# Optimization experiments

Hardware: AMD Instinct MI355X
Metric: run time of the kernel (lower is better)

## Reference

```python
import jax, jax.numpy as jnp
import numpy as np
from jax import lax

NUM_ITER = 10
SMOOTH = 1.0
CL_WEIGHT = 0.5


def _min_pool(x, wh, ww):
    # torch: -max_pool2d(-x) pads with -inf -> min-pool with +inf boundary
    return lax.reduce_window(x, jnp.inf, lax.min,
                             (1, 1, wh, ww), (1, 1, 1, 1),
                             [(0, 0), (0, 0), (wh // 2, wh // 2), (ww // 2, ww // 2)])


def _max_pool(x, wh, ww):
    return lax.reduce_window(x, -jnp.inf, lax.max,
                             (1, 1, wh, ww), (1, 1, 1, 1),
                             [(0, 0), (0, 0), (wh // 2, wh // 2), (ww // 2, ww // 2)])


def soft_erode(img):
    return jnp.minimum(_min_pool(img, 3, 1), _min_pool(img, 1, 3))


def soft_dilate(img):
    return _max_pool(img, 3, 3)


def soft_open(img):
    return soft_dilate(soft_erode(img))


def soft_skeleton(img, num_iter=NUM_ITER):
    # img: (B,1,H,W)
    skel = jax.nn.relu(img - soft_open(img))

    def body(i, carry):
        img_e, skel = carry
        img_e = soft_erode(img_e)
        delta = jax.nn.relu(img_e - soft_open(img_e))
        skel = skel + jax.nn.relu(delta - skel * delta)
        return (img_e, skel)

    _, skel = lax.fori_loop(0, num_iter, body, (img, skel))
    return skel


def soft_dice(pred, target, smooth=SMOOTH):
    inter = jnp.sum(pred * target)
    return (2.0 * inter + smooth) / (jnp.sum(pred) + jnp.sum(target) + smooth)


def setup_inputs() -> dict:
    key = jax.random.key(0)
    k1, k2 = jax.random.split(key)
    pred = jax.random.normal(k1, (8, 1, 1024, 1024), dtype=jnp.float32)
    target = jax.random.randint(k2, (8, 1, 1024, 1024), 0, 2, dtype=jnp.int32)
    return {"pred": pred, "target": target}


def reference(pred, target):
    pred_prob = jax.nn.sigmoid(pred)          # (B,1,H,W)
    target_f = target.astype(pred_prob.dtype)

    skel_pred = soft_skeleton(pred_prob)
    skel_target = soft_skeleton(target_f)

    tprec = (jnp.sum(skel_pred * target_f) + SMOOTH) / (jnp.sum(skel_pred) + SMOOTH)
    tsens = (jnp.sum(skel_target * pred_prob) + SMOOTH) / (jnp.sum(skel_target) + SMOOTH)
    cl_dice = 2.0 * tprec * tsens / (tprec + tsens + 1e-7)

    dice = soft_dice(pred_prob, target_f)
    combined = (1.0 - CL_WEIGHT) * dice + CL_WEIGHT * cl_dice
    loss = 1.0 - combined
    return loss
```

## Files before the change

### kernel.cpp

```cpp
#include <hip/hip_runtime.h>
#include <math.h>

#define IMG  1024
#define TILE 64
#define HALO 12
#define SPP  52
#define NPRED (90*SPP)
#define SEN2 0x40004000u

typedef _Float16 h2 __attribute__((ext_vector_type(2)));
union UH { unsigned u; h2 h; };
__device__ __forceinline__ h2 u2h(unsigned u){ UH x; x.u=u; return x.h; }
__device__ __forceinline__ unsigned h2u(h2 h){ UH x; x.h=h; return x.u; }
__device__ __forceinline__ h2 pmin(h2 a, h2 b){ return __builtin_elementwise_min(a,b); }
__device__ __forceinline__ h2 pmax(h2 a, h2 b){ return __builtin_elementwise_max(a,b); }
__device__ __forceinline__ h2 funnel(h2 hi_src, h2 lo_src){
  return u2h((h2u(lo_src)>>16) | (h2u(hi_src)<<16));
}
__device__ __forceinline__ float sigmoidf(float x){ return 1.0f/(1.0f+__expf(-x)); }
__device__ __forceinline__ h2 unsent(h2 x, h2 onev, h2 zerov){
  h2 t = pmax(x-onev, zerov); return x - t - t;
}
__device__ __forceinline__ unsigned extract8(unsigned w0, unsigned w1, unsigned w2, int bp){
  unsigned long long lo = (unsigned long long)w0 | ((unsigned long long)w1<<32);
  unsigned long long hi = (unsigned long long)w1 | ((unsigned long long)w2<<32);
  unsigned a = (unsigned)(lo >> bp);
  unsigned b = (unsigned)(hi >> (bp & 31));
  return ((bp < 32) ? a : b) & 0xFFu;
}
__device__ __forceinline__ uint4 erode5(uint4 rm, uint4 rc, uint4 rn, h2 lw, h2 rv){
  h2 a0=u2h(rc.x), a1=u2h(rc.y), a2=u2h(rc.z), a3=u2h(rc.w);
  h2 v0=pmin(u2h(rm.x), u2h(rn.x));
  h2 v1=pmin(u2h(rm.y), u2h(rn.y));
  h2 v2=pmin(u2h(rm.z), u2h(rn.z));
  h2 v3=pmin(u2h(rm.w), u2h(rn.w));
  h2 f0=funnel(a0,lw), f1=funnel(a1,a0), f2=funnel(a2,a1), f3=funnel(a3,a2), f4=funnel(rv,a3);
  uint4 e;
  e.x=h2u(pmin(pmin(f0,f1),pmin(v0,a0)));
  e.y=h2u(pmin(pmin(f1,f2),pmin(v1,a1)));
  e.z=h2u(pmin(pmin(f2,f3),pmin(v2,a2)));
  e.w=h2u(pmin(pmin(f3,f4),pmin(v3,a3)));
  return e;
}

template<bool BND>
__device__ void pipeline(const float* __restrict__ pred, const int* __restrict__ targ,
                         long base, int gr0, int gc0, int tid,
                         unsigned* A, unsigned* B, unsigned* Ta, unsigned* Tb,
                         h2 val[8], h2 skel[8], unsigned &tbits, unsigned &skbits) {
  for (int i = tid; i < 104; i += 256) {
    int r = (i < 52) ? 0 : 89, c = (i < 52) ? i : i - 52;
    A[r*SPP + c] = SEN2;  B[r*SPP + c] = SEN2;
  }
  for (int i = tid; i < 704; i += 256) {
    int r = 1 + (i >> 3), w = i & 7;
    w = (w < 2) ? w : 44 + w;
    A[r*SPP + w] = SEN2;  B[r*SPP + w] = SEN2;
  }
  if (!BND) {
    #pragma unroll
    for (int k=0;k<4;++k){
      int u = tid + (k<<8);
      if (u < 968){
        int r = u/11, q = u - r*11;
        long g = base + (long)(gr0+r)*IMG + gc0 + (q<<3);
        float4 pa = *(const float4*)(pred+g);
        float4 pb = *(const float4*)(pred+g+4);
        h2 w0 = {(_Float16)sigmoidf(pa.x), (_Float16)sigmoidf(pa.y)};
        h2 w1 = {(_Float16)sigmoidf(pa.z), (_Float16)sigmoidf(pa.w)};
        h2 w2 = {(_Float16)sigmoidf(pb.x), (_Float16)sigmoidf(pb.y)};
        h2 w3 = {(_Float16)sigmoidf(pb.z), (_Float16)sigmoidf(pb.w)};
        int o = (1+r)*SPP + 2 + (q<<2);
        uint2 d0; d0.x=h2u(w0); d0.y=h2u(w1);
        uint2 d1; d1.x=h2u(w2); d1.y=h2u(w3);
        *(uint2*)&A[o]   = d0;
        *(uint2*)&A[o+2] = d1;
      }
    }
    #pragma unroll
    for (int k=0;k<2;++k){
      int u = tid + (k<<8);
      if (u < 264){
        int r = u/3, w = u - r*3;
        long g = base + (long)(gr0+r)*IMG + gc0 + (w<<5);
        unsigned bits = 0;
        #pragma unroll
        for (int i=0;i<8;++i){
          if (w < 2 || i < 6) {
            int4 tv = *(const int4*)(targ + g + (i<<2));
            unsigned nib = (unsigned)(tv.x!=0) | ((unsigned)(tv.y!=0)<<1)
                         | ((unsigned)(tv.z!=0)<<2) | ((unsigned)(tv.w!=0)<<3);
            bits |= nib << (i<<2);
          }
        }
        if (w==2) bits |= 0xFF000000u;
        Ta[u] = bits;
      }
    }
  } else {
    for (int i=tid; i<88*44; i+=256){
      int r = i/44, wd = i - r*44;
      int gr = gr0 + r;
      bool rok = (unsigned)gr < (unsigned)IMG;
      int gca = gc0 + (wd<<1), gcb = gca + 1;
      _Float16 va = (_Float16)2.0f, vb = (_Float16)2.0f;
      if (rok && (unsigned)gca < (unsigned)IMG) va = (_Float16)sigmoidf(pred[base + (long)gr*IMG + gca]);
      if (rok && (unsigned)gcb < (unsigned)IMG) vb = (_Float16)sigmoidf(pred[base + (long)gr*IMG + gcb]);
      h2 w; w.x = va; w.y = vb;
      A[(1+r)*SPP + 2 + wd] = h2u(w);
    }
    for (int u=tid; u<264; u+=256){
      int r = u/3, w = u - r*3;
      int gr = gr0 + r;
      bool rok = (unsigned)gr < (unsigned)IMG;
      unsigned bits = 0;
      for (int b=0;b<32;++b){
        int c = (w<<5) + b;
        unsigned bit = 1;
        if (c < 88) {
          int gc = gc0 + c;
          if (rok && (unsigned)gc < (unsigned)IMG) bit = (unsigned)(targ[base+(long)gr*IMG+gc] != 0);
        }
        bits |= bit << b;
      }
      Ta[u] = bits;
    }
  }
  __syncthreads();

  unsigned cm0=~0u, cm1=~0u, cm2=0x00FFFFFFu;
  bool colO = false;
  if (BND) {
    int lo = (-gc0 > 0) ? -gc0 : 0;
    int hi = (IMG - gc0 < 88) ? (IMG - gc0) : 88;
    colO = (lo > 0) || (hi < 88);
    unsigned m[3];
    #pragma unroll
    for (int w=0; w<3; ++w){
      int l = lo - (w<<5); if (l<0) l=0;
      int h = hi - (w<<5); if (h>32) h=32;
      unsigned mm = 0;
      if (h > l) {
        unsigned top = (h>=32)? ~0u : ((1u<<h)-1u);
        unsigned bot = (l<=0)? 0u : ((1u<<l)-1u);
        mm = top & ~bot;
      }
      m[w]=mm;
    }
    cm0=m[0]; cm1=m[1]; cm2=m[2] & 0x00FFFFFF;
  }

  const bool eact0 = (tid < 216);
  const int es = tid / 12, eq = tid - es*12;
  const int s5 = es * 5;
  const int ew = eq << 2;
  const int c_lo = (eq<<3) + 3;
  const int c_hi = (eq<<3) - 4;
  const int to = 3 + tid;
  const int twd = tid - (tid/3)*3;
  const bool tex = (tid < 2);
  const int to2 = 259 + tid;
  const int twd2 = (256+tid) - ((256+tid)/3)*3;

  const int qc = tid & 7;
  const int rg = tid >> 3;
  const int r0 = HALO + (rg<<1);
  const int wq = 8 + (qc<<2);
  const int bp = 12 + (qc<<3);

  h2 ep[8];
  {
    uint4 a0 = *(const uint4*)&A[(r0+1)*SPP + wq];
    uint4 a1 = *(const uint4*)&A[(r0+2)*SPP + wq];
    ep[0]=u2h(a0.x); ep[1]=u2h(a0.y); ep[2]=u2h(a0.z); ep[3]=u2h(a0.w);
    ep[4]=u2h(a1.x); ep[5]=u2h(a1.y); ep[6]=u2h(a1.z); ep[7]=u2h(a1.w);
    #pragma unroll
    for (int i=0;i<8;++i){ val[i]=ep[i]; skel[i]=(h2)(_Float16)0.0f; }
  }
  {
    int oa = r0*3, ob = (r0+1)*3;
    tbits = extract8(Ta[oa],Ta[oa+1],Ta[oa+2],bp)
          | (extract8(Ta[ob],Ta[ob+1],Ta[ob+2],bp) << 8);
  }
  unsigned tp0=0,tp1=0,tp2=0, sk0=0,sk1=0,sk2=0;
  const bool td = (tid < 64);
  const int tro = (12 + tid)*3;
  if (td) { tp0=Ta[tro]; tp1=Ta[tro+1]; tp2=Ta[tro+2]; }

  const h2 onev  = {(_Float16)1.0f,(_Float16)1.0f};
  const h2 zerov = {(_Float16)0.0f,(_Float16)0.0f};

  for (int j=0;j<11;++j){
    const bool act = eact0 && (s5+4 >= j+1) && (s5 <= 86-j)
                           && (c_lo >= j+1) && (c_hi <= 86-j);
    if (act){
      uint4 rm = *(const uint4*)&A[s5*SPP + ew];
      uint4 rc = *(const uint4*)&A[(s5+1)*SPP + ew];
      #pragma unroll
      for (int t=0;t<5;++t){
        int brn = s5 + 2 + t; brn = (brn > 89) ? 89 : brn;
        uint4 rn = *(const uint4*)&A[brn*SPP + ew];
        int brc = s5 + 1 + t; brc = (brc > 89) ? 89 : brc;
        h2 lw = u2h(A[brc*SPP + ew - 1]);
        h2 rv = u2h(A[brc*SPP + ew + 4]);
        *(uint4*)&B[brc*SPP + ew] = erode5(rm, rc, rn, lw, rv);
        rm = rc; rc = rn;
      }
    }
    {
      unsigned own=Ta[to], up=Ta[to-3], dn=Ta[to+3];
      unsigned le = (twd>0)? Ta[to-1] : ~0u;
      unsigned ri = (twd<2)? Ta[to+1] : ~0u;
      unsigned h = own & ((own>>1)|(ri<<31)) & ((own<<1)|(le>>31));
      Tb[to] = h & up & dn;
    }
    if (tex){
      unsigned own=Ta[to2], up=Ta[to2-3], dn=Ta[to2+3];
      unsigned le = (twd2>0)? Ta[to2-1] : ~0u;
      unsigned ri = (twd2<2)? Ta[to2+1] : ~0u;
      unsigned h = own & ((own>>1)|(ri<<31)) & ((own<<1)|(le>>31));
      Tb[to2] = h & up & dn;
    }
    __syncthreads();

    if (BND) {
      if (gr0 < 0) {
        for (int i=tid;i<12*44;i+=256){ int r=i/44; B[(1+r)*SPP+2+(i-r*44)] = SEN2; }
        if (tid < 36) Tb[tid] = ~0u;
      }
      if (gr0 + 88 > IMG) {
        for (int i=tid;i<12*44;i+=256){ int r=i/44; B[(77+r)*SPP+2+(i-r*44)] = SEN2; }
        if (tid < 36) Tb[228+tid] = ~0u;
      }
      if (colO) {
        if (gc0 < 0)
          for (int i=tid;i<88*6;i+=256){ int r=i/6; B[(1+r)*SPP+2+(i-r*6)] = SEN2; }
        if (gc0 + 88 > IMG)
          for (int i=tid;i<88*6;i+=256){ int r=i/6; B[(1+r)*SPP+40+(i-r*6)] = SEN2; }
        for (int i=tid;i<264;i+=256){
          int r=i/3, w=i-r*3;
          unsigned nm = (w==0)?~cm0:((w==1)?~cm1:~cm2);
          Tb[i] |= nm;
        }
      }
      __syncthreads();
    }

    h2 H[4][4];
    uint4 cap0, cap1;
    #pragma unroll
    for (int k=0;k<4;++k){
      int ro = (r0+k)*SPP + wq;
      uint4 c = *(const uint4*)&B[ro];
      h2 lwv = u2h(B[ro-1]);
      h2 rwv = u2h(B[ro+4]);
      if (k==1) cap0 = c;
      if (k==2) cap1 = c;
      h2 a0=u2h(c.x),a1=u2h(c.y),a2=u2h(c.z),a3=u2h(c.w);
      if (BND){
        a0=unsent(a0,onev,zerov); a1=unsent(a1,onev,zerov);
        a2=unsent(a2,onev,zerov); a3=unsent(a3,onev,zerov);
        lwv=unsent(lwv,onev,zerov); rwv=unsent(rwv,onev,zerov);
      }
      h2 f0=funnel(a0,lwv), f1=funnel(a1,a0), f2=funnel(a2,a1), f3=funnel(a3,a2), f4=funnel(rwv,a3);
      H[k][0]=pmax(pmax(f0,f1),a0);
      H[k][1]=pmax(pmax(f1,f2),a1);
      H[k][2]=pmax(pmax(f2,f3),a2);
      H[k][3]=pmax(pmax(f3,f4),a3);
    }
    #pragma unroll
    for (int i=0;i<4;++i){
      h2 m0 = pmax(pmax(H[0][i],H[1][i]),H[2][i]);
      h2 m1 = pmax(pmax(H[1][i],H[2][i]),H[3][i]);
      h2 d0 = pmax(ep[i]-m0, zerov);
      h2 d1 = pmax(ep[4+i]-m1, zerov);
      h2 x0 = d0 - skel[i]*d0;
      h2 x1 = d1 - skel[4+i]*d1;
      skel[i]   = skel[i]   + pmax(x0, zerov);
      skel[4+i] = skel[4+i] + pmax(x1, zerov);
    }
    ep[0]=u2h(cap0.x); ep[1]=u2h(cap0.y); ep[2]=u2h(cap0.z); ep[3]=u2h(cap0.w);
    ep[4]=u2h(cap1.x); ep[5]=u2h(cap1.y); ep[6]=u2h(cap1.z); ep[7]=u2h(cap1.w);

    if (td) {
      unsigned o0=Tb[tro], o1=Tb[tro+1], o2=Tb[tro+2];
      unsigned u0=Tb[tro-3], u1=Tb[tro-2], u2=Tb[tro-1];
      unsigned n0=Tb[tro+3], n1=Tb[tro+4], n2=Tb[tro+5];
      unsigned v0,v1,v2;
      if (BND){
        unsigned mu = ((unsigned)(gr0 + 11 + tid) < (unsigned)IMG) ? ~0u : 0u;
        unsigned md = ((unsigned)(gr0 + 13 + tid) < (unsigned)IMG) ? ~0u : 0u;
        v0 = ((u0&mu)|o0|(n0&md)) & cm0;
        v1 = ((u1&mu)|o1|(n1&md)) & cm1;
        v2 = ((u2&mu)|o2|(n2&md)) & cm2;
      } else {
        v0 = u0|o0|n0; v1 = u1|o1|n1; v2 = u2|o2|n2;
      }
      unsigned d0 = v0 | (v0<<1) | (v0>>1) | (v1<<31);
      unsigned d1 = v1 | (v1<<1) | (v0>>31) | (v1>>1) | (v2<<31);
      unsigned d2 = v2 | (v2<<1) | (v1>>31) | (v2>>1);
      sk0 |= tp0 & ~d0;
      sk1 |= tp1 & ~d1;
      sk2 |= tp2 & ~d2;
      tp0 = o0; tp1 = o1; tp2 = o2;
    }
    unsigned* t1 = A;  A = B;  B = t1;
    unsigned* t2 = Ta; Ta = Tb; Tb = t2;
  }

  __syncthreads();
  if (td){ Ta[3*tid]=sk0; Ta[3*tid+1]=sk1; Ta[3*tid+2]=sk2; }
  __syncthreads();
  {
    int o = (r0-12)*3;
    skbits = extract8(Ta[o],Ta[o+1],Ta[o+2],bp)
           | (extract8(Ta[o+3],Ta[o+4],Ta[o+5],bp) << 8);
  }
}

__global__ __launch_bounds__(256,4)
void cl_dice_main(const float* __restrict__ pred, const int* __restrict__ targ,
                  float* __restrict__ ws) {
  __shared__ alignas(16) unsigned sPA[NPRED];
  __shared__ alignas(16) unsigned sPB[NPRED];
  __shared__ unsigned sTA[264], sTB[264];
  const int tid = threadIdx.x;
  const int gr0 = blockIdx.y * TILE - HALO;
  const int gc0 = blockIdx.x * TILE - HALO;
  const long base = (long)blockIdx.z * (long)(IMG * IMG);

  h2 val[8], skel[8]; unsigned tbits, skbits;
  const bool bnd = (blockIdx.x == 0) | (blockIdx.x == gridDim.x - 1) |
                   (blockIdx.y == 0) | (blockIdx.y == gridDim.y - 1);
  if (!bnd) pipeline<false>(pred, targ, base, gr0, gc0, tid, sPA, sPB, sTA, sTB, val, skel, tbits, skbits);
  else      pipeline<true >(pred, targ, base, gr0, gc0, tid, sPA, sPB, sTA, sTB, val, skel, tbits, skbits);

  float s[7] = {0,0,0,0,0,0,0};
  #pragma unroll
  for (int k=0;k<8;++k){
    int bb = ((k>>2)<<3) + ((k&3)<<1);
    float p0=(float)val[k].x,  p1=(float)val[k].y;
    float a0=(float)skel[k].x, a1=(float)skel[k].y;
    float t0=(float)((tbits>>bb)&1u),  t1=(float)((tbits>>(bb+1))&1u);
    float b0=(float)((skbits>>bb)&1u), b1=(float)((skbits>>(bb+1))&1u);
    s[0]+=a0+a1;        s[1]+=a0*t0+a1*t1;
    s[2]+=b0+b1;        s[3]+=b0*p0+b1*p1;
    s[4]+=p0*t0+p1*t1;  s[5]+=p0+p1;  s[6]+=t0+t1;
  }

  float* red = (float*)sPA;
  #pragma unroll
  for (int k=0;k<7;++k){
    float v = s[k];
    v += __shfl_down(v,32); v += __shfl_down(v,16); v += __shfl_down(v,8);
    v += __shfl_down(v,4);  v += __shfl_down(v,2);  v += __shfl_down(v,1);
    if ((tid & 63) == 0) red[(tid>>6)*8 + k] = v;
  }
  __syncthreads();
  if (tid < 7) {
    float v = red[tid] + red[8+tid] + red[16+tid] + red[24+tid];
    int blk = (blockIdx.z * gridDim.y + blockIdx.y) * gridDim.x + blockIdx.x;
    ws[blk*8 + tid] = v;
  }
}

__global__ __launch_bounds__(256)
void cl_dice_finalize(const float* __restrict__ ws, float* __restrict__ out, int nblk) {
  __shared__ float red[4][8];
  int tid = threadIdx.x;
  float acc[7] = {0,0,0,0,0,0,0};
  for (int i=tid; i<nblk; i+=256) {
    #pragma unroll
    for (int k=0;k<7;++k) acc[k] += ws[i*8 + k];
  }
  #pragma unroll
  for (int k=0;k<7;++k){
    float v = acc[k];
    v += __shfl_down(v,32); v += __shfl_down(v,16); v += __shfl_down(v,8);
    v += __shfl_down(v,4);  v += __shfl_down(v,2);  v += __shfl_down(v,1);
    if ((tid & 63) == 0) red[tid>>6][k] = v;
  }
  __syncthreads();
  if (tid == 0) {
    float t0[7];
    #pragma unroll
    for (int k=0;k<7;++k) t0[k] = red[0][k] + red[1][k] + red[2][k] + red[3][k];
    float sum_sp = t0[0], sum_spt = t0[1], sum_st = t0[2], sum_stp = t0[3];
    float inter  = t0[4], sum_p   = t0[5], sum_t  = t0[6];
    float tprec = (sum_spt + 1.0f) / (sum_sp + 1.0f);
    float tsens = (sum_stp + 1.0f) / (sum_st + 1.0f);
    float cl    = 2.0f * tprec * tsens / (tprec + tsens + 1e-7f);
    float dice  = (2.0f * inter + 1.0f) / (sum_p + sum_t + 1.0f);
    out[0] = 1.0f - 0.5f * (dice + cl);
  }
}

extern "C" void kernel_launch(void* const* d_in, const int* in_sizes, int n_in,
                              void* d_out, int out_size, void* d_ws, size_t ws_size,
                              hipStream_t stream) {
  const float* pred = (const float*)d_in[0];
  const int*   targ = (const int*)d_in[1];
  float* ws  = (float*)d_ws;
  float* out = (float*)d_out;

  const int B = in_sizes[0] / (IMG * IMG);
  dim3 grid(IMG / TILE, IMG / TILE, B);
  cl_dice_main<<<grid, 256, 0, stream>>>(pred, targ, ws);

  const int nblk = (IMG / TILE) * (IMG / TILE) * B;
  cl_dice_finalize<<<1, 256, 0, stream>>>(ws, out, nblk);
}
```

Baseline: 243.4 us.

## Double block size to 512 threads and halve per-thread work in skeleton pipeline

Moves from 256 to 512 threads per tile block. Each thread now erodes 2-row strips instead of 5-row strips, and computes the open/skeleton update for one row of 8 pixels instead of two. Target bit-erosion is spread over more threads. The aim is more latency hiding and a shorter per-thread critical path per iteration, at the cost of more redundant halo loads, more LDS traffic and heavier barriers.

```diff
diff --git a/kernel.cpp b/kernel.cpp
--- a/kernel.cpp
+++ b/kernel.cpp
@@ -47,20 +47,20 @@
 __device__ void pipeline(const float* __restrict__ pred, const int* __restrict__ targ,
                          long base, int gr0, int gc0, int tid,
                          unsigned* A, unsigned* B, unsigned* Ta, unsigned* Tb,
-                         h2 val[8], h2 skel[8], unsigned &tbits, unsigned &skbits) {
-  for (int i = tid; i < 104; i += 256) {
+                         h2 val[4], h2 skel[4], unsigned &tbits, unsigned &skbits) {
+  for (int i = tid; i < 104; i += 512) {
     int r = (i < 52) ? 0 : 89, c = (i < 52) ? i : i - 52;
     A[r*SPP + c] = SEN2;  B[r*SPP + c] = SEN2;
   }
-  for (int i = tid; i < 704; i += 256) {
+  for (int i = tid; i < 704; i += 512) {
     int r = 1 + (i >> 3), w = i & 7;
     w = (w < 2) ? w : 44 + w;
     A[r*SPP + w] = SEN2;  B[r*SPP + w] = SEN2;
   }
   if (!BND) {
     #pragma unroll
-    for (int k=0;k<4;++k){
-      int u = tid + (k<<8);
+    for (int k=0;k<2;++k){
+      int u = tid + (k<<9);
       if (u < 968){
         int r = u/11, q = u - r*11;
         long g = base + (long)(gr0+r)*IMG + gc0 + (q<<3);
@@ -77,28 +77,25 @@
         *(uint2*)&A[o+2] = d1;
       }
     }
-    #pragma unroll
-    for (int k=0;k<2;++k){
-      int u = tid + (k<<8);
-      if (u < 264){
-        int r = u/3, w = u - r*3;
-        long g = base + (long)(gr0+r)*IMG + gc0 + (w<<5);
-        unsigned bits = 0;
-        #pragma unroll
-        for (int i=0;i<8;++i){
-          if (w < 2 || i < 6) {
-            int4 tv = *(const int4*)(targ + g + (i<<2));
-            unsigned nib = (unsigned)(tv.x!=0) | ((unsigned)(tv.y!=0)<<1)
-                         | ((unsigned)(tv.z!=0)<<2) | ((unsigned)(tv.w!=0)<<3);
-            bits |= nib << (i<<2);
-          }
+    if (tid < 264){
+      int u = tid;
+      int r = u/3, w = u - r*3;
+      long g = base + (long)(gr0+r)*IMG + gc0 + (w<<5);
+      unsigned bits = 0;
+      #pragma unroll
+      for (int i=0;i<8;++i){
+        if (w < 2 || i < 6) {
+          int4 tv = *(const int4*)(targ + g + (i<<2));
+          unsigned nib = (unsigned)(tv.x!=0) | ((unsigned)(tv.y!=0)<<1)
+                       | ((unsigned)(tv.z!=0)<<2) | ((unsigned)(tv.w!=0)<<3);
+          bits |= nib << (i<<2);
         }
-        if (w==2) bits |= 0xFF000000u;
-        Ta[u] = bits;
-      }
+      }
+      if (w==2) bits |= 0xFF000000u;
+      Ta[u] = bits;
     }
   } else {
-    for (int i=tid; i<88*44; i+=256){
+    for (int i=tid; i<88*44; i+=512){
       int r = i/44, wd = i - r*44;
       int gr = gr0 + r;
       bool rok = (unsigned)gr < (unsigned)IMG;
@@ -109,7 +106,7 @@
       h2 w; w.x = va; w.y = vb;
       A[(1+r)*SPP + 2 + wd] = h2u(w);
     }
-    for (int u=tid; u<264; u+=256){
+    for (int u=tid; u<264; u+=512){
       int r = u/3, w = u - r*3;
       int gr = gr0 + r;
       bool rok = (unsigned)gr < (unsigned)IMG;
@@ -150,37 +147,37 @@
     cm0=m[0]; cm1=m[1]; cm2=m[2] & 0x00FFFFFF;
   }
 
-  const bool eact0 = (tid < 216);
-  const int es = tid / 12, eq = tid - es*12;
-  const int s5 = es * 5;
-  const int ew = eq << 2;
-  const int c_lo = (eq<<3) + 3;
-  const int c_hi = (eq<<3) - 4;
-  const int to = 3 + tid;
-  const int twd = tid - (tid/3)*3;
-  const bool tex = (tid < 2);
-  const int to2 = 259 + tid;
-  const int twd2 = (256+tid) - ((256+tid)/3)*3;
+  const int es  = tid / 12,  eq  = tid - es*12;
+  const int s2  = es*2;
+  const int ew  = eq << 2;
+  const int cl1 = (eq<<3) + 3;
+  const int ch1 = (eq<<3) - 4;
+  const bool has2 = (tid < 16);
+  const int u2  = 512 + tid;
+  const int es2 = u2/12, eq2 = u2 - es2*12;
+  const int s2b = es2*2, ew2 = eq2<<2;
+  const int cl2 = (eq2<<3)+3, ch2 = (eq2<<3)-4;
+
+  const bool tex = (tid < 258);
+  const int  to  = 3 + tid;
+  const int  twd = tid % 3;
 
   const int qc = tid & 7;
   const int rg = tid >> 3;
-  const int r0 = HALO + (rg<<1);
+  const int pr = HALO + rg;
   const int wq = 8 + (qc<<2);
   const int bp = 12 + (qc<<3);
 
-  h2 ep[8];
+  h2 ep[4];
   {
-    uint4 a0 = *(const uint4*)&A[(r0+1)*SPP + wq];
-    uint4 a1 = *(const uint4*)&A[(r0+2)*SPP + wq];
+    uint4 a0 = *(const uint4*)&A[(pr+1)*SPP + wq];
     ep[0]=u2h(a0.x); ep[1]=u2h(a0.y); ep[2]=u2h(a0.z); ep[3]=u2h(a0.w);
-    ep[4]=u2h(a1.x); ep[5]=u2h(a1.y); ep[6]=u2h(a1.z); ep[7]=u2h(a1.w);
-    #pragma unroll
-    for (int i=0;i<8;++i){ val[i]=ep[i]; skel[i]=(h2)(_Float16)0.0f; }
+    #pragma unroll
+    for (int i=0;i<4;++i){ val[i]=ep[i]; skel[i]=(h2)(_Float16)0.0f; }
   }
   {
-    int oa = r0*3, ob = (r0+1)*3;
-    tbits = extract8(Ta[oa],Ta[oa+1],Ta[oa+2],bp)
-          | (extract8(Ta[ob],Ta[ob+1],Ta[ob+2],bp) << 8);
+    int oa = pr*3;
+    tbits = extract8(Ta[oa],Ta[oa+1],Ta[oa+2],bp);
   }
   unsigned tp0=0,tp1=0,tp2=0, sk0=0,sk1=0,sk2=0;
   const bool td = (tid < 64);
@@ -191,53 +188,49 @@
   const h2 zerov = {(_Float16)0.0f,(_Float16)0.0f};
 
   for (int j=0;j<11;++j){
-    const bool act = eact0 && (s5+4 >= j+1) && (s5 <= 86-j)
-                           && (c_lo >= j+1) && (c_hi <= 86-j);
-    if (act){
-      uint4 rm = *(const uint4*)&A[s5*SPP + ew];
-      uint4 rc = *(const uint4*)&A[(s5+1)*SPP + ew];
-      #pragma unroll
-      for (int t=0;t<5;++t){
-        int brn = s5 + 2 + t; brn = (brn > 89) ? 89 : brn;
-        uint4 rn = *(const uint4*)&A[brn*SPP + ew];
-        int brc = s5 + 1 + t; brc = (brc > 89) ? 89 : brc;
-        h2 lw = u2h(A[brc*SPP + ew - 1]);
-        h2 rv = u2h(A[brc*SPP + ew + 4]);
-        *(uint4*)&B[brc*SPP + ew] = erode5(rm, rc, rn, lw, rv);
-        rm = rc; rc = rn;
-      }
-    }
     {
+      auto ERO = [&](int s2_, int ew_){
+        uint4 rm = *(const uint4*)&A[s2_*SPP + ew_];
+        uint4 rc = *(const uint4*)&A[(s2_+1)*SPP + ew_];
+        #pragma unroll
+        for (int t=0;t<2;++t){
+          uint4 rn = *(const uint4*)&A[(s2_+2+t)*SPP + ew_];
+          int brc = s2_+1+t;
+          h2 lw = u2h(A[brc*SPP + ew_ - 1]);
+          h2 rv = u2h(A[brc*SPP + ew_ + 4]);
+          *(uint4*)&B[brc*SPP + ew_] = erode5(rm, rc, rn, lw, rv);
+          rm = rc; rc = rn;
+        }
+      };
+      if ((s2+1 >= j+1) && (s2 <= 86-j) && (cl1 >= j+1) && (ch1 <= 86-j))
+        ERO(s2, ew);
+      if (has2 && (s2b+1 >= j+1) && (s2b <= 86-j) && (cl2 >= j+1) && (ch2 <= 86-j))
+        ERO(s2b, ew2);
+    }
+    if (tex){
       unsigned own=Ta[to], up=Ta[to-3], dn=Ta[to+3];
       unsigned le = (twd>0)? Ta[to-1] : ~0u;
       unsigned ri = (twd<2)? Ta[to+1] : ~0u;
       unsigned h = own & ((own>>1)|(ri<<31)) & ((own<<1)|(le>>31));
       Tb[to] = h & up & dn;
     }
-    if (tex){
-      unsigned own=Ta[to2], up=Ta[to2-3], dn=Ta[to2+3];
-      unsigned le = (twd2>0)? Ta[to2-1] : ~0u;
-      unsigned ri = (twd2<2)? Ta[to2+1] : ~0u;
-      unsigned h = own & ((own>>1)|(ri<<31)) & ((own<<1)|(le>>31));
-      Tb[to2] = h & up & dn;
-    }
     __syncthreads();
 
     if (BND) {
       if (gr0 < 0) {
-        for (int i=tid;i<12*44;i+=256){ int r=i/44; B[(1+r)*SPP+2+(i-r*44)] = SEN2; }
+        for (int i=tid;i<12*44;i+=512){ int r=i/44; B[(1+r)*SPP+2+(i-r*44)] = SEN2; }
         if (tid < 36) Tb[tid] = ~0u;
       }
       if (gr0 + 88 > IMG) {
-        for (int i=tid;i<12*44;i+=256){ int r=i/44; B[(77+r)*SPP+2+(i-r*44)] = SEN2; }
+        for (int i=tid;i<12*44;i+=512){ int r=i/44; B[(77+r)*SPP+2+(i-r*44)] = SEN2; }
         if (tid < 36) Tb[228+tid] = ~0u;
       }
       if (colO) {
         if (gc0 < 0)
-          for (int i=tid;i<88*6;i+=256){ int r=i/6; B[(1+r)*SPP+2+(i-r*6)] = SEN2; }
+          for (int i=tid;i<88*6;i+=512){ int r=i/6; B[(1+r)*SPP+2+(i-r*6)] = SEN2; }
         if (gc0 + 88 > IMG)
-          for (int i=tid;i<88*6;i+=256){ int r=i/6; B[(1+r)*SPP+40+(i-r*6)] = SEN2; }
-        for (int i=tid;i<264;i+=256){
+          for (int i=tid;i<88*6;i+=512){ int r=i/6; B[(1+r)*SPP+40+(i-r*6)] = SEN2; }
+        for (int i=tid;i<264;i+=512){
           int r=i/3, w=i-r*3;
           unsigned nm = (w==0)?~cm0:((w==1)?~cm1:~cm2);
           Tb[i] |= nm;
@@ -246,45 +239,41 @@
       __syncthreads();
     }
 
-    h2 H[4][4];
-    uint4 cap0, cap1;
-    #pragma unroll
-    for (int k=0;k<4;++k){
-      int ro = (r0+k)*SPP + wq;
-      uint4 c = *(const uint4*)&B[ro];
-      h2 lwv = u2h(B[ro-1]);
-      h2 rwv = u2h(B[ro+4]);
-      if (k==1) cap0 = c;
-      if (k==2) cap1 = c;
-      h2 a0=u2h(c.x),a1=u2h(c.y),a2=u2h(c.z),a3=u2h(c.w);
-      if (BND){
-        a0=unsent(a0,onev,zerov); a1=unsent(a1,onev,zerov);
-        a2=unsent(a2,onev,zerov); a3=unsent(a3,onev,zerov);
-        lwv=unsent(lwv,onev,zerov); rwv=unsent(rwv,onev,zerov);
-      }
-      h2 f0=funnel(a0,lwv), f1=funnel(a1,a0), f2=funnel(a2,a1), f3=funnel(a3,a2), f4=funnel(rwv,a3);
-      H[k][0]=pmax(pmax(f0,f1),a0);
-      H[k][1]=pmax(pmax(f1,f2),a1);
-      H[k][2]=pmax(pmax(f2,f3),a2);
-      H[k][3]=pmax(pmax(f3,f4),a3);
-    }
-    #pragma unroll
-    for (int i=0;i<4;++i){
-      h2 m0 = pmax(pmax(H[0][i],H[1][i]),H[2][i]);
-      h2 m1 = pmax(pmax(H[1][i],H[2][i]),H[3][i]);
-      h2 d0 = pmax(ep[i]-m0, zerov);
-      h2 d1 = pmax(ep[4+i]-m1, zerov);
-      h2 x0 = d0 - skel[i]*d0;
-      h2 x1 = d1 - skel[4+i]*d1;
-      skel[i]   = skel[i]   + pmax(x0, zerov);
-      skel[4+i] = skel[4+i] + pmax(x1, zerov);
-    }
-    ep[0]=u2h(cap0.x); ep[1]=u2h(cap0.y); ep[2]=u2h(cap0.z); ep[3]=u2h(cap0.w);
-    ep[4]=u2h(cap1.x); ep[5]=u2h(cap1.y); ep[6]=u2h(cap1.z); ep[7]=u2h(cap1.w);
+    {
+      h2 H[3][4];
+      uint4 cap;
+      #pragma unroll
+      for (int k=0;k<3;++k){
+        int ro = (pr+k)*SPP + wq;
+        uint4 c = *(const uint4*)&B[ro];
+        h2 lwv = u2h(B[ro-1]);
+        h2 rwv = u2h(B[ro+4]);
+        if (k==1) cap = c;
+        h2 a0=u2h(c.x),a1=u2h(c.y),a2=u2h(c.z),a3=u2h(c.w);
+        if (BND){
+          a0=unsent(a0,onev,zerov); a1=unsent(a1,onev,zerov);
+          a2=unsent(a2,onev,zerov); a3=unsent(a3,onev,zerov);
+          lwv=unsent(lwv,onev,zerov); rwv=unsent(rwv,onev,zerov);
+        }
+        h2 f0=funnel(a0,lwv), f1=funnel(a1,a0), f2=funnel(a2,a1), f3=funnel(a3,a2), f4=funnel(rwv,a3);
+        H[k][0]=pmax(pmax(f0,f1),a0);
+        H[k][1]=pmax(pmax(f1,f2),a1);
+        H[k][2]=pmax(pmax(f2,f3),a2);
+        H[k][3]=pmax(pmax(f3,f4),a3);
+      }
+      #pragma unroll
+      for (int i=0;i<4;++i){
+        h2 m0 = pmax(pmax(H[0][i],H[1][i]),H[2][i]);
+        h2 d0 = pmax(ep[i]-m0, zerov);
+        h2 x0 = d0 - skel[i]*d0;
+        skel[i] = skel[i] + pmax(x0, zerov);
+      }
+      ep[0]=u2h(cap.x); ep[1]=u2h(cap.y); ep[2]=u2h(cap.z); ep[3]=u2h(cap.w);
+    }
 
     if (td) {
       unsigned o0=Tb[tro], o1=Tb[tro+1], o2=Tb[tro+2];
-      unsigned u0=Tb[tro-3], u1=Tb[tro-2], u2=Tb[tro-1];
+      unsigned u0=Tb[tro-3], u1=Tb[tro-2], u2v=Tb[tro-1];
       unsigned n0=Tb[tro+3], n1=Tb[tro+4], n2=Tb[tro+5];
       unsigned v0,v1,v2;
       if (BND){
@@ -292,9 +281,9 @@
         unsigned md = ((unsigned)(gr0 + 13 + tid) < (unsigned)IMG) ? ~0u : 0u;
         v0 = ((u0&mu)|o0|(n0&md)) & cm0;
         v1 = ((u1&mu)|o1|(n1&md)) & cm1;
-        v2 = ((u2&mu)|o2|(n2&md)) & cm2;
+        v2 = ((u2v&mu)|o2|(n2&md)) & cm2;
       } else {
-        v0 = u0|o0|n0; v1 = u1|o1|n1; v2 = u2|o2|n2;
+        v0 = u0|o0|n0; v1 = u1|o1|n1; v2 = u2v|o2|n2;
       }
       unsigned d0 = v0 | (v0<<1) | (v0>>1) | (v1<<31);
       unsigned d1 = v1 | (v1<<1) | (v0>>31) | (v1>>1) | (v2<<31);
@@ -312,13 +301,12 @@
   if (td){ Ta[3*tid]=sk0; Ta[3*tid+1]=sk1; Ta[3*tid+2]=sk2; }
   __syncthreads();
   {
-    int o = (r0-12)*3;
-    skbits = extract8(Ta[o],Ta[o+1],Ta[o+2],bp)
-           | (extract8(Ta[o+3],Ta[o+4],Ta[o+5],bp) << 8);
-  }
-}
-
-__global__ __launch_bounds__(256,4)
+    int o = rg*3;
+    skbits = extract8(Ta[o],Ta[o+1],Ta[o+2],bp);
+  }
+}
+
+__global__ __launch_bounds__(512,8)
 void cl_dice_main(const float* __restrict__ pred, const int* __restrict__ targ,
                   float* __restrict__ ws) {
   __shared__ alignas(16) unsigned sPA[NPRED];
@@ -329,7 +317,7 @@
   const int gc0 = blockIdx.x * TILE - HALO;
   const long base = (long)blockIdx.z * (long)(IMG * IMG);
 
-  h2 val[8], skel[8]; unsigned tbits, skbits;
+  h2 val[4], skel[4]; unsigned tbits, skbits;
   const bool bnd = (blockIdx.x == 0) | (blockIdx.x == gridDim.x - 1) |
                    (blockIdx.y == 0) | (blockIdx.y == gridDim.y - 1);
   if (!bnd) pipeline<false>(pred, targ, base, gr0, gc0, tid, sPA, sPB, sTA, sTB, val, skel, tbits, skbits);
@@ -337,8 +325,8 @@
 
   float s[7] = {0,0,0,0,0,0,0};
   #pragma unroll
-  for (int k=0;k<8;++k){
-    int bb = ((k>>2)<<3) + ((k&3)<<1);
+  for (int k=0;k<4;++k){
+    int bb = k<<1;
     float p0=(float)val[k].x,  p1=(float)val[k].y;
     float a0=(float)skel[k].x, a1=(float)skel[k].y;
     float t0=(float)((tbits>>bb)&1u),  t1=(float)((tbits>>(bb+1))&1u);
@@ -358,7 +346,9 @@
   }
   __syncthreads();
   if (tid < 7) {
-    float v = red[tid] + red[8+tid] + red[16+tid] + red[24+tid];
+    float v = 0.f;
+    #pragma unroll
+    for (int w8=0; w8<8; ++w8) v += red[w8*8 + tid];
     int blk = (blockIdx.z * gridDim.y + blockIdx.y) * gridDim.x + blockIdx.x;
     ws[blk*8 + tid] = v;
   }
@@ -405,7 +395,7 @@
 
   const int B = in_sizes[0] / (IMG * IMG);
   dim3 grid(IMG / TILE, IMG / TILE, B);
-  cl_dice_main<<<grid, 256, 0, stream>>>(pred, targ, ws);
+  cl_dice_main<<<grid, 512, 0, stream>>>(pred, targ, ws);
 
   const int nblk = (IMG / TILE) * (IMG / TILE) * B;
   cl_dice_finalize<<<1, 256, 0, stream>>>(ws, out, nblk);
```

Result: slower. 251.9 us (+3.5%).
